# Kernel optimization log

Hardware: AMD Instinct MI355X
Metric: run time of the kernel (lower is better)

Reference implementation:

```python
import jax, jax.numpy as jnp
import numpy as np

C = 64          # num_channels
NB = 8          # num_bessel
NE = 10         # num_elements
N_NODES = 20000
N_EDGES = 320000

def _silu_norm():
    # e3nn normalize2mom constant for silu: 1/sqrt(E[silu(Z)^2]), Z~N(0,1)
    x, w = np.polynomial.hermite.hermgauss(100)
    z = np.sqrt(2.0) * x
    f = z / (1.0 + np.exp(-z))
    m2 = float(np.sum(w * f * f) / np.sqrt(np.pi))
    return np.float32(1.0 / np.sqrt(m2))

C_SILU = _silu_norm()
SQRT3 = np.float32(np.sqrt(3.0))
SQRT2 = np.float32(np.sqrt(2.0))
INV_SQRT_C = np.float32(1.0 / np.sqrt(C))
INV_SQRT_2C = np.float32(1.0 / np.sqrt(2 * C))
INV_SQRT_3C = np.float32(1.0 / np.sqrt(3 * C))
INV_SQRT_NB = np.float32(1.0 / np.sqrt(NB))
INV_SQRT_64 = np.float32(1.0 / np.sqrt(64.0))


def setup_inputs() -> dict:
    key = jax.random.key(0)
    ks = jax.random.split(key, 22)
    n = lambda k, s: jax.random.normal(k, s, dtype=jnp.float32)
    return {
        "node_feats": n(ks[0], (N_NODES, 4 * C)),
        "edge_feats": jax.random.uniform(ks[1], (N_EDGES, NB), dtype=jnp.float32),
        "edge_attrs": n(ks[2], (N_EDGES, 4)),
        "iedges": jax.random.randint(ks[3], (N_EDGES,), 0, N_NODES),
        "jedges": jax.random.randint(ks[4], (N_EDGES,), 0, N_NODES),
        "atomic_numbers": jax.random.randint(ks[5], (N_NODES,), 0, NE),
        "Wup0": n(ks[6], (C, C)), "Wup1": n(ks[7], (C, C)),
        "Wm1": n(ks[8], (NB, 64)), "Wm2": n(ks[9], (64, 64)),
        "Wm3": n(ks[10], (64, 64)), "Wm4": n(ks[11], (64, 5 * C)),
        "Wl0": n(ks[12], (2 * C, C)), "Wl1": n(ks[13], (3 * C, C)),
        "Ws0c1": n(ks[14], (NE, 1, C)), "Ws0c2": n(ks[15], (NE, 2, C)),
        "Ws0c3": n(ks[16], (NE, 2, C)),
        "Ws1c1": n(ks[17], (NE, 1, C)), "Ws1c2": n(ks[18], (NE, 1, C)),
        "Ws1c3": n(ks[19], (NE, 2, C)),
        "Wp0": n(ks[20], (C, C)), "Wp1": n(ks[21], (C, C)),
    }


def reference(node_feats, edge_feats, edge_attrs, iedges, jedges, atomic_numbers,
              Wup0, Wup1, Wm1, Wm2, Wm3, Wm4, Wl0, Wl1,
              Ws0c1, Ws0c2, Ws0c3, Ws1c1, Ws1c2, Ws1c3, Wp0, Wp1):
    Nn = node_feats.shape[0]
    # split irreps: C scalars (0e) then C vectors (1e), channel-major layout
    s = node_feats[:, :C]                       # (N, C)
    v = node_feats[:, C:].reshape(Nn, C, 3)     # (N, C, 3)

    # linear_up: per-l channel mixing, fan-in normalized (e3nn o3.Linear)
    s = (s @ Wup0) * INV_SQRT_C
    v = jnp.einsum('ncm,ck->nkm', v, Wup1) * INV_SQRT_C

    # conv_tp_weights: e3nn FullyConnectedNet [8,64,64,64,5C] with silu
    h = jax.nn.silu(edge_feats @ (Wm1 * INV_SQRT_NB)) * C_SILU
    h = jax.nn.silu(h @ (Wm2 * INV_SQRT_64)) * C_SILU
    h = jax.nn.silu(h @ (Wm3 * INV_SQRT_64)) * C_SILU
    tpw = h @ (Wm4 * INV_SQRT_64)               # (E, 5C)

    # gather sender node features per edge
    xs = s[iedges]                              # (E, C)
    xv = v[iedges]                              # (E, C, 3)
    eas = edge_attrs[:, 0:1]                    # (E, 1) scalar edge attr
    eav = edge_attrs[:, 1:4]                    # (E, 3) vector edge attr

    # 5 uvu CG paths (component-normalized e3nn TensorProduct):
    wa, wb = tpw[:, 0:C], tpw[:, C:2 * C]
    wc, wd, we = tpw[:, 2 * C:3 * C], tpw[:, 3 * C:4 * C], tpw[:, 4 * C:5 * C]
    m0 = wa * xs * eas                                              # 0e x 0e -> 0e
    m1 = wb * jnp.einsum('ecm,em->ec', xv, eav) / SQRT3             # 1e x 1e -> 0e
    m2 = (wc * xs)[:, :, None] * eav[:, None, :]                    # 0e x 1e -> 1e
    m3 = (wd * eas)[:, :, None] * xv                                # 1e x 0e -> 1e
    m4 = we[:, :, None] * jnp.cross(xv, eav[:, None, :]) / SQRT2    # 1e x 1e -> 1e

    # scatter-sum messages to receiver nodes
    msg_s = jax.ops.segment_sum(jnp.concatenate([m0, m1], axis=1), jedges, num_segments=Nn)        # (N, 2C)
    msg_v = jax.ops.segment_sum(jnp.concatenate([m2, m3, m4], axis=1), jedges, num_segments=Nn)    # (N, 3C, 3)

    # linear: middle irreps (2C x 0e + 3C x 1e) -> C x (0e + 1e)
    s2 = (msg_s @ Wl0) * INV_SQRT_2C            # (N, C)
    v2 = jnp.einsum('ncm,ck->nkm', msg_v, Wl1) * INV_SQRT_3C  # (N, C, 3)

    # symmetric (ACE/MACE) contraction, correlation=3, element-dependent weights
    w01 = Ws0c1[atomic_numbers, 0]              # (N, C)
    w02 = Ws0c2[atomic_numbers]                 # (N, 2, C)
    w03 = Ws0c3[atomic_numbers]                 # (N, 2, C)
    w11 = Ws1c1[atomic_numbers, 0]
    w12 = Ws1c2[atomic_numbers, 0]
    w13 = Ws1c3[atomic_numbers]
    vv = jnp.sum(v2 * v2, axis=-1)              # (N, C) = |v|^2 per channel
    out_s = (w01 * s2 + w02[:, 0] * s2 * s2 + w02[:, 1] * vv / SQRT3
             + w03[:, 0] * s2 * s2 * s2 + w03[:, 1] * s2 * vv / SQRT3)
    coef_v = w11 + w12 * s2 + w13[:, 0] * s2 * s2 + w13[:, 1] * vv / SQRT3
    out_v = coef_v[:, :, None] * v2             # (N, C, 3)

    # linearproduct
    so = (out_s @ Wp0) * INV_SQRT_C
    vo = jnp.einsum('ncm,ck->nkm', out_v, Wp1) * INV_SQRT_C
    return jnp.concatenate([so, vo.reshape(Nn, 3 * C)], axis=1)   # (N, 4C)
```

## Files before the change

### kernel.cpp

```cpp
#include <hip/hip_runtime.h>


typedef unsigned short u16;
typedef unsigned int u32;
typedef __attribute__((ext_vector_type(8))) short bf16x8;
typedef __attribute__((ext_vector_type(4))) float f32x4;

#define CW_UP0 0
#define CW_UP1 4096
#define CW_M1  8192
#define CW_M2  8704
#define CW_M3  12800
#define CW_M4  16896
#define CW_L0  37376
#define CW_L1  45568
#define CW_P0  57856
#define CW_P1  61952
#define CW_S01 66048
#define CW_S02 66688
#define CW_S03 67968
#define CW_S11 69248
#define CW_S12 69888
#define CW_S13 70528
#define CW_TOTAL 71808

#define C_SILU     1.6765224f
#define INV_SQRT3  0.57735027f
#define INV_SQRT2  0.70710678f
#define SC_L1      0.35355339f
#define SC_L234    0.125f

#define HS16 72
#define NFRAG 116
#define FW0 60
#define FW1 76
#define FP0 100
#define FP1 108
#define TP 88

__device__ __forceinline__ float b2f(u16 u) {
  union { u32 i; float f; } x; x.i = ((u32)u) << 16; return x.f;
}
__device__ __forceinline__ u16 f2b(float f) {
  union { float f; u32 i; } x; x.f = f;
  u32 i = x.i;
  u32 r = (i + 0x7fffu + ((i >> 16) & 1u)) >> 16;
  return (u16)r;
}
__device__ __forceinline__ float ldf(const void* p, size_t i, int f32) {
  return f32 ? ((const float*)p)[i] : b2f(((const u16*)p)[i]);
}
__device__ __forceinline__ float silu_n(float x) {
  return C_SILU * x / (1.0f + __expf(-x));
}

__global__ void k_detect(const void* nf, int* flag) {
  __shared__ int cnt;
  if (threadIdx.x == 0) cnt = 0;
  __syncthreads();
  const u16* p = (const u16*)nf;
  int wild = 0;
  for (int i = threadIdx.x; i < 4096; i += 256) {
    float ax = fabsf(b2f(p[i]));
    if (!(ax <= 1e10f) || (ax != 0.f && ax < 1e-10f)) wild++;
  }
  atomicAdd(&cnt, wild);
  __syncthreads();
  if (threadIdx.x == 0) *flag = (cnt > 100) ? 1 : 0;
}

struct WPtrs { const void* p[16]; };

__global__ __launch_bounds__(256) void k_front(
    WPtrs wp, float* __restrict__ cw, u16* __restrict__ bwH,
    u16* __restrict__ bwL, const int* __restrict__ je, int* __restrict__ deg,
    const void* __restrict__ nf, float* __restrict__ sup,
    float* __restrict__ vup, int nN, int nE, int nb0,
    const int* __restrict__ flagp) {
  __shared__ float row[4][256];
  const int f32 = *flagp;
  int bid = blockIdx.x, tid = threadIdx.x;

  if (bid < 281) {
    const int   sizes[16]  = {4096,4096,512,4096,4096,20480,8192,12288,4096,
                              4096,640,1280,1280,640,640,1280};
    const float scales[16] = {0.125f,0.125f,0.35355339f,0.125f,0.125f,0.125f,
                              0.08838835f,0.07216878f,0.125f,0.125f,
                              1.f,1.f,1.f,1.f,1.f,1.f};
    int gid = bid * 256 + tid;
    if (gid >= CW_TOTAL) return;
    int off = gid, seg = 0;
    while (off >= sizes[seg]) { off -= sizes[seg]; seg++; }
    cw[gid] = ldf(wp.p[seg], off, f32) * scales[seg];
  } else if (bid < 513) {
    int gid = (bid - 281) * 256 + tid;
    int f = gid >> 9, idx = gid & 511;
    int l = idx >> 3, j = idx & 7;
    int q = l >> 4, col16 = l & 15;
    float v = 0.f;
    if (f < 4) {
      int k = q * 8 + j, n = f * 16 + col16;
      if (k < 8) v = ldf(wp.p[2], (size_t)k * 64 + n, f32);
    } else if (f < 20) {
      const void* w = (f < 12) ? wp.p[3] : wp.p[4];
      int t = (f < 12) ? f - 4 : f - 12;
      int n = (t >> 1) * 16 + col16, ks = t & 1;
      int k = ks * 32 + q * 8 + j;
      v = ldf(w, (size_t)k * 64 + n, f32);
    } else if (f < 60) {
      int t = f - 20;
      int n = (t >> 1) * 16 + col16, ks = t & 1;
      int k = ks * 32 + q * 8 + j;
      v = ldf(wp.p[5], (size_t)k * 320 + n, f32);
    } else if (f < 76) {
      int t = f - FW0, ks = t >> 2, n = t & 3;
      int k = ks * 32 + q * 8 + j;
      v = ldf(wp.p[6], (size_t)k * 64 + n * 16 + col16, f32) * 0.08838835f;
    } else if (f < 100) {
      int t = f - FW1, ks = t >> 2, n = t & 3;
      int k = ks * 32 + q * 8 + j;
      v = ldf(wp.p[7], (size_t)k * 64 + n * 16 + col16, f32) * 0.07216878f;
    } else if (f < 108) {
      int t = f - FP0, ks = t >> 2, n = t & 3;
      int k = ks * 32 + q * 8 + j;
      v = ldf(wp.p[8], (size_t)k * 64 + n * 16 + col16, f32) * 0.125f;
    } else {
      int t = f - FP1, ks = t >> 2, n = t & 3;
      int k = ks * 32 + q * 8 + j;
      v = ldf(wp.p[9], (size_t)k * 64 + n * 16 + col16, f32) * 0.125f;
    }
    u16 hi = f2b(v);
    u16 lo = f2b(v - b2f(hi));
    size_t o = (size_t)f * 512 + (size_t)l * 8 + j;
    bwH[o] = hi;
    bwL[o] = lo;
  } else if (bid < nb0) {
    int e = (bid - 513) * 256 + tid;
    if (e < nE) atomicAdd(&deg[je[e]], 1);
  } else {
    int w = tid >> 6, l = tid & 63;
    int n = (bid - nb0) * 4 + w;
    bool valid = n < nN;
    int nn = valid ? n : 0;
#pragma unroll
    for (int t = 0; t < 4; t++)
      row[w][t * 64 + l] = ldf(nf, (size_t)nn * 256 + t * 64 + l, f32);
    __syncthreads();
    float sacc = 0.f, v0 = 0.f, v1 = 0.f, v2 = 0.f;
#pragma unroll 8
    for (int c = 0; c < 64; c++) {
      float w0 = ldf(wp.p[0], (size_t)c * 64 + l, f32);
      float w1 = ldf(wp.p[1], (size_t)c * 64 + l, f32);
      sacc += row[w][c] * w0;
      v0 += row[w][64 + c * 3 + 0] * w1;
      v1 += row[w][64 + c * 3 + 1] * w1;
      v2 += row[w][64 + c * 3 + 2] * w1;
    }
    if (valid) {
      sup[(size_t)n * 64 + l] = sacc * 0.125f;
      vup[((size_t)n * 3 + 0) * 64 + l] = v0 * 0.125f;
      vup[((size_t)n * 3 + 1) * 64 + l] = v1 * 0.125f;
      vup[((size_t)n * 3 + 2) * 64 + l] = v2 * 0.125f;
    }
  }
}

__global__ __launch_bounds__(256) void k_scan(const int* __restrict__ deg,
                                              int* __restrict__ offs,
                                              int* __restrict__ cursor, int nN) {
  __shared__ int part[256];
  int t = threadIdx.x;
  int per = (nN + 255) / 256;
  int lo = t * per, hi = (t + 1) * per; if (hi > nN) hi = nN;
  int s = 0;
  for (int i = lo; i < hi; i++) s += deg[i];
  part[t] = s;
  __syncthreads();
  if (t == 0) {
    int run = 0;
    for (int i = 0; i < 256; i++) { int v = part[i]; part[i] = run; run += v; }
    offs[nN] = run;
  }
  __syncthreads();
  int run = part[t];
  for (int i = lo; i < hi; i++) {
    offs[i] = run; cursor[i] = run; run += deg[i];
  }
}

__global__ __launch_bounds__(256) void k_scatter2(
    const int* __restrict__ je, const int* __restrict__ ie,
    const void* __restrict__ ea, const void* __restrict__ ef,
    int* __restrict__ cursor, int* __restrict__ iSlot,
    float4* __restrict__ eaSlot, float4* __restrict__ efSlot, int nE,
    const int* __restrict__ flagp) {
  const int f32 = *flagp;
  int e = blockIdx.x * 256 + threadIdx.x;
  if (e >= nE) return;
  int pos = atomicAdd(&cursor[je[e]], 1);
  iSlot[pos] = ie[e];
  float4 av;
  float4 f0, f1;
  if (f32) {
    av = ((const float4*)ea)[e];
    f0 = ((const float4*)ef)[(size_t)e * 2];
    f1 = ((const float4*)ef)[(size_t)e * 2 + 1];
  } else {
    uint2 r = ((const uint2*)ea)[e];
    av = make_float4(b2f(r.x & 0xffff), b2f(r.x >> 16),
                     b2f(r.y & 0xffff), b2f(r.y >> 16));
    uint4 u = ((const uint4*)ef)[e];
    f0 = make_float4(b2f(u.x & 0xffff), b2f(u.x >> 16),
                     b2f(u.y & 0xffff), b2f(u.y >> 16));
    f1 = make_float4(b2f(u.z & 0xffff), b2f(u.z >> 16),
                     b2f(u.w & 0xffff), b2f(u.w >> 16));
  }
  eaSlot[pos] = av;
  efSlot[(size_t)pos * 2] = f0;
  efSlot[(size_t)pos * 2 + 1] = f1;
}

__global__ __launch_bounds__(192) void k_mlp4(
    const float4* __restrict__ efSlot, const int* __restrict__ offs,
    const u16* __restrict__ bwH, const u16* __restrict__ bwL,
    u16* __restrict__ tpw, int gn0, int gn1, int capEff) {
  __shared__ u16 H[3][64 * HS16];
  int tid = threadIdx.x;
  int w = tid >> 6, l = tid & 63;
  int m = l & 15, q = l >> 4;
  int base = offs[gn0];
  int cnt = offs[gn1] - base;
  int lim = cnt < capEff ? cnt : capEff;
  int tb = (blockIdx.x * 3 + w) * 64;
  if (tb >= lim) return;
  u16* Hw = H[w];

  bf16x8 zero8 = {0,0,0,0,0,0,0,0};
  bf16x8 A1h[4], A1l[4];
#pragma unroll
  for (int t = 0; t < 4; t++) { A1h[t] = zero8; A1l[t] = zero8; }
  if (q == 0) {
#pragma unroll
    for (int t = 0; t < 4; t++) {
      int s = tb + t * 16 + m; if (s > lim - 1) s = lim - 1;
      float4 q0 = efSlot[((size_t)(base + s)) * 2];
      float4 q1 = efSlot[((size_t)(base + s)) * 2 + 1];
      float v[8] = {q0.x, q0.y, q0.z, q0.w, q1.x, q1.y, q1.z, q1.w};
      bf16x8 hi, lo;
#pragma unroll
      for (int j = 0; j < 8; j++) {
        u16 h = f2b(v[j]);
        hi[j] = (short)h;
        lo[j] = (short)f2b(v[j] - b2f(h));
      }
      A1h[t] = hi; A1l[t] = lo;
    }
  }
#pragma unroll
  for (int n = 0; n < 4; n++) {
    bf16x8 Bh = *(const bf16x8*)(bwH + (size_t)n * 512 + (size_t)l * 8);
    bf16x8 Bl = *(const bf16x8*)(bwL + (size_t)n * 512 + (size_t)l * 8);
#pragma unroll
    for (int t = 0; t < 4; t++) {
      f32x4 c = (f32x4){0.f, 0.f, 0.f, 0.f};
      c = __builtin_amdgcn_mfma_f32_16x16x32_bf16(A1h[t], Bh, c, 0, 0, 0);
      c = __builtin_amdgcn_mfma_f32_16x16x32_bf16(A1l[t], Bh, c, 0, 0, 0);
      c = __builtin_amdgcn_mfma_f32_16x16x32_bf16(A1h[t], Bl, c, 0, 0, 0);
#pragma unroll
      for (int r = 0; r < 4; r++)
        Hw[(t * 16 + q * 4 + r) * HS16 + n * 16 + m] =
            f2b(silu_n(c[r] * SC_L1));
    }
  }

#pragma unroll
  for (int layer = 0; layer < 2; layer++) {
    int fragBase = 4 + layer * 8;
    bf16x8 Ah[2][4];
#pragma unroll
    for (int ks = 0; ks < 2; ks++)
#pragma unroll
      for (int t = 0; t < 4; t++)
        Ah[ks][t] = *(const bf16x8*)(Hw + (t * 16 + m) * HS16 + ks * 32 + q * 8);
#pragma unroll
    for (int n = 0; n < 4; n++) {
      bf16x8 B0h = *(const bf16x8*)(bwH + (size_t)(fragBase + n * 2 + 0) * 512 +
                                    (size_t)l * 8);
      bf16x8 B0l = *(const bf16x8*)(bwL + (size_t)(fragBase + n * 2 + 0) * 512 +
                                    (size_t)l * 8);
      bf16x8 B1h = *(const bf16x8*)(bwH + (size_t)(fragBase + n * 2 + 1) * 512 +
                                    (size_t)l * 8);
      bf16x8 B1l = *(const bf16x8*)(bwL + (size_t)(fragBase + n * 2 + 1) * 512 +
                                    (size_t)l * 8);
#pragma unroll
      for (int t = 0; t < 4; t++) {
        f32x4 c = (f32x4){0.f, 0.f, 0.f, 0.f};
        c = __builtin_amdgcn_mfma_f32_16x16x32_bf16(Ah[0][t], B0h, c, 0, 0, 0);
        c = __builtin_amdgcn_mfma_f32_16x16x32_bf16(Ah[0][t], B0l, c, 0, 0, 0);
        c = __builtin_amdgcn_mfma_f32_16x16x32_bf16(Ah[1][t], B1h, c, 0, 0, 0);
        c = __builtin_amdgcn_mfma_f32_16x16x32_bf16(Ah[1][t], B1l, c, 0, 0, 0);
#pragma unroll
        for (int r = 0; r < 4; r++)
          Hw[(t * 16 + q * 4 + r) * HS16 + n * 16 + m] =
              f2b(silu_n(c[r] * SC_L234));
      }
    }
  }

  {
    bf16x8 Ah[2][4];
#pragma unroll
    for (int ks = 0; ks < 2; ks++)
#pragma unroll
      for (int t = 0; t < 4; t++)
        Ah[ks][t] = *(const bf16x8*)(Hw + (t * 16 + m) * HS16 + ks * 32 + q * 8);
    for (int c4 = 0; c4 < 5; c4++) {
#pragma unroll
      for (int nn2 = 0; nn2 < 4; nn2++) {
        int n = c4 * 4 + nn2;
        bf16x8 B0h = *(const bf16x8*)(bwH + (size_t)(20 + n * 2 + 0) * 512 +
                                      (size_t)l * 8);
        bf16x8 B0l = *(const bf16x8*)(bwL + (size_t)(20 + n * 2 + 0) * 512 +
                                      (size_t)l * 8);
        bf16x8 B1h = *(const bf16x8*)(bwH + (size_t)(20 + n * 2 + 1) * 512 +
                                      (size_t)l * 8);
        bf16x8 B1l = *(const bf16x8*)(bwL + (size_t)(20 + n * 2 + 1) * 512 +
                                      (size_t)l * 8);
#pragma unroll
        for (int t = 0; t < 4; t++) {
          f32x4 c = (f32x4){0.f, 0.f, 0.f, 0.f};
          c = __builtin_amdgcn_mfma_f32_16x16x32_bf16(Ah[0][t], B0h, c, 0, 0, 0);
          c = __builtin_amdgcn_mfma_f32_16x16x32_bf16(Ah[0][t], B0l, c, 0, 0, 0);
          c = __builtin_amdgcn_mfma_f32_16x16x32_bf16(Ah[1][t], B1h, c, 0, 0, 0);
          c = __builtin_amdgcn_mfma_f32_16x16x32_bf16(Ah[1][t], B1l, c, 0, 0, 0);
#pragma unroll
          for (int r = 0; r < 4; r++)
            Hw[(t * 16 + q * 4 + r) * HS16 + nn2 * 16 + m] =
                f2b(c[r] * SC_L234);
        }
      }
      int r8 = l >> 3, cc = l & 7;
#pragma unroll
      for (int i = 0; i < 8; i++) {
        int row = i * 8 + r8;
        int srow = tb + row;
        if (srow < lim) {
          uint4 v = *(const uint4*)(Hw + row * HS16 + cc * 8);
          *(uint4*)(tpw + (size_t)srow * 320 + c4 * 64 + cc * 8) = v;
        }
      }
    }
  }
}

__global__ __launch_bounds__(256) void k_gather6(
    const int* __restrict__ iSlot, const float4* __restrict__ eaSlot,
    const int* __restrict__ offs, const float* __restrict__ sup,
    const float* __restrict__ vup, const u16* __restrict__ tpw,
    u16* __restrict__ msgSh, u16* __restrict__ msgSl,
    u16* __restrict__ msgVh, u16* __restrict__ msgVl,
    int gn0, int gn1, int capEff) {
  int w = threadIdx.x >> 6, l = threadIdx.x & 63;
  int n = gn0 + blockIdx.x * 4 + w;
  if (n >= gn1) return;
  int gbase = offs[gn0];
  int start = offs[n];
  int deg = offs[n + 1] - start;
  int avail = capEff - (start - gbase);
  int dmax = deg < avail ? deg : avail;
  if (dmax < 0) dmax = 0;

  float as0 = 0.f, as1 = 0.f;
  float av[9];
#pragma unroll
  for (int m = 0; m < 9; m++) av[m] = 0.f;

  for (int c0 = 0; c0 < dmax; c0 += 64) {
    int rem = dmax - c0;
    int cend = rem < 64 ? rem : 64;
    int iA = 0;
    float4 eaA = make_float4(0.f, 0.f, 0.f, 0.f);
    if (l < cend) {
      iA = iSlot[start + c0 + l];
      eaA = eaSlot[start + c0 + l];
    }
    for (int qq = 0; qq < cend; qq++) {
      int i = __shfl(iA, qq);
      float eas = __shfl(eaA.x, qq);
      float ev0 = __shfl(eaA.y, qq);
      float ev1 = __shfl(eaA.z, qq);
      float ev2 = __shfl(eaA.w, qq);
      const u16* tp = tpw + (size_t)(start - gbase + c0 + qq) * 320;
      float wa  = b2f(tp[l]);
      float wbv = b2f(tp[64 + l]);
      float wc  = b2f(tp[128 + l]);
      float wd  = b2f(tp[192 + l]);
      float we_ = b2f(tp[256 + l]);
      float xs  = sup[(size_t)i * 64 + l];
      float xv0 = vup[((size_t)i * 3 + 0) * 64 + l];
      float xv1 = vup[((size_t)i * 3 + 1) * 64 + l];
      float xv2 = vup[((size_t)i * 3 + 2) * 64 + l];
      float dot = xv0 * ev0 + xv1 * ev1 + xv2 * ev2;
      as0 += wa * xs * eas;
      as1 += wbv * dot * INV_SQRT3;
      float wcxs = wc * xs;
      float wde  = wd * eas;
      float wef  = we_ * INV_SQRT2;
      av[0] += wcxs * ev0; av[1] += wcxs * ev1; av[2] += wcxs * ev2;
      av[3] += wde * xv0;  av[4] += wde * xv1;  av[5] += wde * xv2;
      av[6] += wef * (xv1 * ev2 - xv2 * ev1);
      av[7] += wef * (xv2 * ev0 - xv0 * ev2);
      av[8] += wef * (xv0 * ev1 - xv1 * ev0);
    }
  }

  {
    u16 h0 = f2b(as0), h1 = f2b(as1);
    msgSh[(size_t)n * 128 + l] = h0;
    msgSh[(size_t)n * 128 + 64 + l] = h1;
    msgSl[(size_t)n * 128 + l] = f2b(as0 - b2f(h0));
    msgSl[(size_t)n * 128 + 64 + l] = f2b(as1 - b2f(h1));
  }
#pragma unroll
  for (int c = 0; c < 3; c++) {
#pragma unroll
    for (int b = 0; b < 3; b++) {
      float x = av[b * 3 + c];
      u16 h = f2b(x);
      size_t o = (size_t)n * 576 + c * 192 + b * 64 + l;
      msgVh[o] = h;
      msgVl[o] = f2b(x - b2f(h));
    }
  }
}

__global__ __launch_bounds__(256) void k_post2(
    const u16* __restrict__ msgSh, const u16* __restrict__ msgSl,
    const u16* __restrict__ msgVh, const u16* __restrict__ msgVl,
    const int* __restrict__ an, const float* __restrict__ cw,
    const u16* __restrict__ bwH, const u16* __restrict__ bwL,
    void* __restrict__ out, int nN, const int* __restrict__ flagp) {
  __shared__ u16 Thi[16][TP];
  __shared__ u16 Tlo[16][TP];
  const int f32 = *flagp;
  int tid = threadIdx.x;
  int w = tid >> 6, l = tid & 63;
  int m = l & 15, q = l >> 4;
  int n0 = blockIdx.x * 16;
  int rowA = n0 + m; if (rowA > nN - 1) rowA = nN - 1;

  f32x4 s2 = (f32x4){0.f, 0.f, 0.f, 0.f};
#pragma unroll
  for (int ks = 0; ks < 4; ks++) {
    bf16x8 Bh = *(const bf16x8*)(bwH + (size_t)(FW0 + ks * 4 + w) * 512 +
                                 (size_t)l * 8);
    bf16x8 Bl = *(const bf16x8*)(bwL + (size_t)(FW0 + ks * 4 + w) * 512 +
                                 (size_t)l * 8);
    bf16x8 Ah = *(const bf16x8*)(msgSh + (size_t)rowA * 128 + ks * 32 + q * 8);
    bf16x8 Al = *(const bf16x8*)(msgSl + (size_t)rowA * 128 + ks * 32 + q * 8);
    s2 = __builtin_amdgcn_mfma_f32_16x16x32_bf16(Ah, Bh, s2, 0, 0, 0);
    s2 = __builtin_amdgcn_mfma_f32_16x16x32_bf16(Al, Bh, s2, 0, 0, 0);
    s2 = __builtin_amdgcn_mfma_f32_16x16x32_bf16(Ah, Bl, s2, 0, 0, 0);
  }

  f32x4 v2[3];
#pragma unroll
  for (int c = 0; c < 3; c++) v2[c] = (f32x4){0.f, 0.f, 0.f, 0.f};
#pragma unroll
  for (int ks = 0; ks < 6; ks++) {
    bf16x8 Bh = *(const bf16x8*)(bwH + (size_t)(FW1 + ks * 4 + w) * 512 +
                                 (size_t)l * 8);
    bf16x8 Bl = *(const bf16x8*)(bwL + (size_t)(FW1 + ks * 4 + w) * 512 +
                                 (size_t)l * 8);
#pragma unroll
    for (int c = 0; c < 3; c++) {
      size_t o = (size_t)rowA * 576 + c * 192 + ks * 32 + q * 8;
      bf16x8 Ah = *(const bf16x8*)(msgVh + o);
      bf16x8 Al = *(const bf16x8*)(msgVl + o);
      v2[c] = __builtin_amdgcn_mfma_f32_16x16x32_bf16(Ah, Bh, v2[c], 0, 0, 0);
      v2[c] = __builtin_amdgcn_mfma_f32_16x16x32_bf16(Al, Bh, v2[c], 0, 0, 0);
      v2[c] = __builtin_amdgcn_mfma_f32_16x16x32_bf16(Ah, Bl, v2[c], 0, 0, 0);
    }
  }

  float os[4], ov0[4], ov1[4], ov2[4];
#pragma unroll
  for (int r = 0; r < 4; r++) {
    int node = n0 + q * 4 + r;
    int nc = node > nN - 1 ? nN - 1 : node;
    int a = an[nc];
    int ch = w * 16 + m;
    float s2v = s2[r];
    float va = v2[0][r], vb = v2[1][r], vc = v2[2][r];
    float vv = va * va + vb * vb + vc * vc;
    float w01  = cw[CW_S01 + a * 64 + ch];
    float w02a = cw[CW_S02 + a * 128 + ch];
    float w02b = cw[CW_S02 + a * 128 + 64 + ch];
    float w03a = cw[CW_S03 + a * 128 + ch];
    float w03b = cw[CW_S03 + a * 128 + 64 + ch];
    float w11  = cw[CW_S11 + a * 64 + ch];
    float w12  = cw[CW_S12 + a * 64 + ch];
    float w13a = cw[CW_S13 + a * 128 + ch];
    float w13b = cw[CW_S13 + a * 128 + 64 + ch];
    float s2sq = s2v * s2v;
    float vvs = vv * INV_SQRT3;
    os[r] = w01 * s2v + w02a * s2sq + w02b * vvs + w03a * s2sq * s2v +
            w03b * s2v * vvs;
    float coef = w11 + w12 * s2v + w13a * s2sq + w13b * vvs;
    ov0[r] = coef * va;
    ov1[r] = coef * vb;
    ov2[r] = coef * vc;
  }

#define POST2_G2(SRC, FB, STORE_S, COMP)                                       \
  {                                                                            \
    __syncthreads();                                                           \
    _Pragma("unroll")                                                          \
    for (int r = 0; r < 4; r++) {                                              \
      float x = SRC[r];                                                        \
      u16 h = f2b(x);                                                          \
      Thi[q * 4 + r][w * 16 + m] = h;                                          \
      Tlo[q * 4 + r][w * 16 + m] = f2b(x - b2f(h));                            \
    }                                                                          \
    __syncthreads();                                                           \
    f32x4 d = (f32x4){0.f, 0.f, 0.f, 0.f};                                     \
    _Pragma("unroll")                                                          \
    for (int ks = 0; ks < 2; ks++) {                                           \
      bf16x8 Bh = *(const bf16x8*)(bwH + (size_t)(FB + ks * 4 + w) * 512 +     \
                                   (size_t)l * 8);                             \
      bf16x8 Bl = *(const bf16x8*)(bwL + (size_t)(FB + ks * 4 + w) * 512 +     \
                                   (size_t)l * 8);                             \
      bf16x8 Ah = *(const bf16x8*)(&Thi[m][ks * 32 + q * 8]);                  \
      bf16x8 Al = *(const bf16x8*)(&Tlo[m][ks * 32 + q * 8]);                  \
      d = __builtin_amdgcn_mfma_f32_16x16x32_bf16(Ah, Bh, d, 0, 0, 0);         \
      d = __builtin_amdgcn_mfma_f32_16x16x32_bf16(Al, Bh, d, 0, 0, 0);         \
      d = __builtin_amdgcn_mfma_f32_16x16x32_bf16(Ah, Bl, d, 0, 0, 0);         \
    }                                                                          \
    _Pragma("unroll")                                                          \
    for (int r = 0; r < 4; r++) {                                              \
      int node = n0 + q * 4 + r;                                               \
      if (node < nN) {                                                         \
        int ch = w * 16 + m;                                                   \
        size_t basep = (size_t)node * 256;                                     \
        size_t oidx = STORE_S ? (basep + ch) : (basep + 64 + ch * 3 + COMP);   \
        if (f32) ((float*)out)[oidx] = d[r];                                   \
        else ((u16*)out)[oidx] = f2b(d[r]);                                    \
      }                                                                        \
    }                                                                          \
  }

  POST2_G2(os, FP0, 1, 0)
  POST2_G2(ov0, FP1, 0, 0)
  POST2_G2(ov1, FP1, 0, 1)
  POST2_G2(ov2, FP1, 0, 2)
#undef POST2_G2
}

extern "C" void kernel_launch(void* const* d_in, const int* in_sizes, int n_in,
                              void* d_out, int out_size, void* d_ws,
                              size_t ws_size, hipStream_t stream) {
  const void* nf = d_in[0];
  const void* ef = d_in[1];
  const void* ea = d_in[2];
  const int* ie = (const int*)d_in[3];
  const int* je = (const int*)d_in[4];
  const int* an = (const int*)d_in[5];
  int nN = in_sizes[0] / 256;
  int nE = in_sizes[3];

  size_t intCnt = (size_t)3 * nN + 1 + nE;
  intCnt = (intCnt + 3) & ~(size_t)3;
  int* deg    = (int*)d_ws;
  int* offs   = deg + nN;
  int* cursor = offs + nN + 1;
  int* iSlot  = cursor + nN;
  float* cw   = (float*)d_ws + intCnt;
  float* sup  = cw + CW_TOTAL;
  float* vup  = sup + (size_t)nN * 64;
  int* flag   = (int*)(vup + (size_t)nN * 192);

  size_t msgByte = (size_t)((char*)(flag + 1) - (char*)d_ws);
  msgByte = (msgByte + 15) & ~(size_t)15;
  u16* msgSh = (u16*)((char*)d_ws + msgByte);
  u16* msgSl = msgSh + (size_t)nN * 128;
  u16* msgVh = msgSl + (size_t)nN * 128;
  u16* msgVl = msgVh + (size_t)nN * 576;

  size_t eaByte = msgByte + (size_t)nN * 1408 * 2;
  eaByte = (eaByte + 15) & ~(size_t)15;
  float4* eaSlot = (float4*)((char*)d_ws + eaByte);
  float4* efSlot = eaSlot + nE;
  size_t bwByte = eaByte + (size_t)nE * 16 + (size_t)nE * 32;
  u16* bwH = (u16*)((char*)d_ws + bwByte);
  u16* bwL = bwH + (size_t)NFRAG * 512;
  size_t tpwByte = bwByte + (size_t)NFRAG * 512 * 2 * 2;
  tpwByte = (tpwByte + 15) & ~(size_t)15;
  u16* tpw = (u16*)((char*)d_ws + tpwByte);
  size_t capE = (ws_size > tpwByte) ? (ws_size - tpwByte) / 640 : 0;

  int G = 64;
  int nodesPer = (nN + 63) / 64;
  for (int g = 1; g <= 64; g++) {
    int npg = (nN + g - 1) / g;
    size_t worst = (size_t)npg * nE / nN + 6000;
    if (worst <= capE) { G = g; nodesPer = npg; break; }
  }
  int capEff = (int)((size_t)nodesPer * nE / nN + 6000);
  if ((size_t)capEff > capE) capEff = (int)capE;

  k_detect<<<1, 256, 0, stream>>>(nf, flag);
  hipMemsetAsync(deg, 0, (size_t)nN * sizeof(int), stream);

  WPtrs wp;
  const int widx[16] = {6, 7, 8, 9, 10, 11, 12, 13, 20, 21,
                        14, 15, 16, 17, 18, 19};
  for (int i = 0; i < 16; i++) wp.p[i] = d_in[widx[i]];

  int histNB = (nE + 255) / 256;
  int nb0 = 513 + histNB;
  int nupNB = (nN + 3) / 4;
  k_front<<<nb0 + nupNB, 256, 0, stream>>>(wp, cw, bwH, bwL, je, deg, nf,
                                           sup, vup, nN, nE, nb0, flag);
  k_scan<<<1, 256, 0, stream>>>(deg, offs, cursor, nN);
  k_scatter2<<<(nE + 255) / 256, 256, 0, stream>>>(je, ie, ea, ef, cursor,
                                                   iSlot, eaSlot, efSlot, nE,
                                                   flag);

  for (int g = 0; g < G; g++) {
    int gn0 = g * nodesPer;
    if (gn0 >= nN) break;
    int gn1 = gn0 + nodesPer; if (gn1 > nN) gn1 = nN;
    int mlpBlocks = (capEff + 191) / 192;
    k_mlp4<<<mlpBlocks, 192, 0, stream>>>(efSlot, offs, bwH, bwL, tpw,
                                          gn0, gn1, capEff);
    int gBlocks = (gn1 - gn0 + 3) / 4;
    k_gather6<<<gBlocks, 256, 0, stream>>>(iSlot, eaSlot, offs, sup, vup,
                                           tpw, msgSh, msgSl, msgVh, msgVl,
                                           gn0, gn1, capEff);
  }
  int postNB = (nN + 15) / 16;
  k_post2<<<postNB, 256, 0, stream>>>(msgSh, msgSl, msgVh, msgVl, an, cw,
                                      bwH, bwL, d_out, nN, flag);
}
```

Measured before the change: 500.2 us.

## Fold degree zeroing into detect, stage up-weights in LDS, parallelize scan

Zeroing of the degree array moves into the single-block detect kernel, which removes one memset launch. The linear_up weight matrices are staged into shared memory once per block instead of being read from global memory inside the channel loop. The serial per-thread prefix scan is replaced by a chunked wave-shuffle scan that gives coalesced access. In exchange, k_front now uses about 32KB more LDS per block (which may reduce occupancy), and every block, including the weight-conversion and histogram blocks, declares it. The single-block detect also now zeroes 20k ints on its own.

```diff
diff --git a/kernel.cpp b/kernel.cpp
--- a/kernel.cpp
+++ b/kernel.cpp
@@ -54,7 +54,7 @@
   return C_SILU * x / (1.0f + __expf(-x));
 }
 
-__global__ void k_detect(const void* nf, int* flag) {
+__global__ void k_detect(const void* nf, int* flag, int* deg, int nN) {
   __shared__ int cnt;
   if (threadIdx.x == 0) cnt = 0;
   __syncthreads();
@@ -65,6 +65,7 @@
     if (!(ax <= 1e10f) || (ax != 0.f && ax < 1e-10f)) wild++;
   }
   atomicAdd(&cnt, wild);
+  for (int i = threadIdx.x; i < nN; i += 256) deg[i] = 0;
   __syncthreads();
   if (threadIdx.x == 0) *flag = (cnt > 100) ? 1 : 0;
 }
@@ -78,6 +79,8 @@
     float* __restrict__ vup, int nN, int nE, int nb0,
     const int* __restrict__ flagp) {
   __shared__ float row[4][256];
+  __shared__ float w0s[4096];
+  __shared__ float w1s[4096];
   const int f32 = *flagp;
   int bid = blockIdx.x, tid = threadIdx.x;
 
@@ -143,14 +146,19 @@
     bool valid = n < nN;
     int nn = valid ? n : 0;
 #pragma unroll
+    for (int i = 0; i < 16; i++) {
+      w0s[i * 256 + tid] = ldf(wp.p[0], i * 256 + tid, f32);
+      w1s[i * 256 + tid] = ldf(wp.p[1], i * 256 + tid, f32);
+    }
+#pragma unroll
     for (int t = 0; t < 4; t++)
       row[w][t * 64 + l] = ldf(nf, (size_t)nn * 256 + t * 64 + l, f32);
     __syncthreads();
     float sacc = 0.f, v0 = 0.f, v1 = 0.f, v2 = 0.f;
 #pragma unroll 8
     for (int c = 0; c < 64; c++) {
-      float w0 = ldf(wp.p[0], (size_t)c * 64 + l, f32);
-      float w1 = ldf(wp.p[1], (size_t)c * 64 + l, f32);
+      float w0 = w0s[c * 64 + l];
+      float w1 = w1s[c * 64 + l];
       sacc += row[w][c] * w0;
       v0 += row[w][64 + c * 3 + 0] * w1;
       v1 += row[w][64 + c * 3 + 1] * w1;
@@ -168,24 +176,34 @@
 __global__ __launch_bounds__(256) void k_scan(const int* __restrict__ deg,
                                               int* __restrict__ offs,
                                               int* __restrict__ cursor, int nN) {
-  __shared__ int part[256];
+  __shared__ int wsum[8];
   int t = threadIdx.x;
-  int per = (nN + 255) / 256;
-  int lo = t * per, hi = (t + 1) * per; if (hi > nN) hi = nN;
-  int s = 0;
-  for (int i = lo; i < hi; i++) s += deg[i];
-  part[t] = s;
-  __syncthreads();
-  if (t == 0) {
-    int run = 0;
-    for (int i = 0; i < 256; i++) { int v = part[i]; part[i] = run; run += v; }
-    offs[nN] = run;
-  }
-  __syncthreads();
-  int run = part[t];
-  for (int i = lo; i < hi; i++) {
-    offs[i] = run; cursor[i] = run; run += deg[i];
-  }
+  int lane = t & 63, wv = t >> 6;
+  int base = 0;
+  for (int c0 = 0; c0 < nN; c0 += 256) {
+    int i = c0 + t;
+    int v = (i < nN) ? deg[i] : 0;
+    int s = v;
+#pragma unroll
+    for (int off = 1; off < 64; off <<= 1) {
+      int x = __shfl_up(s, off);
+      if (lane >= off) s += x;
+    }
+    if (lane == 63) wsum[wv] = s;
+    __syncthreads();
+    if (t == 0) {
+      int r = 0;
+#pragma unroll
+      for (int ww = 0; ww < 4; ww++) { int x = wsum[ww]; wsum[ww] = r; r += x; }
+      wsum[4] = r;
+    }
+    __syncthreads();
+    int excl = base + wsum[wv] + s - v;
+    if (i < nN) { offs[i] = excl; cursor[i] = excl; }
+    base += wsum[4];
+    __syncthreads();
+  }
+  if (t == 0) offs[nN] = base;
 }
 
 __global__ __launch_bounds__(256) void k_scatter2(
@@ -608,8 +626,7 @@
   int capEff = (int)((size_t)nodesPer * nE / nN + 6000);
   if ((size_t)capEff > capE) capEff = (int)capE;
 
-  k_detect<<<1, 256, 0, stream>>>(nf, flag);
-  hipMemsetAsync(deg, 0, (size_t)nN * sizeof(int), stream);
+  k_detect<<<1, 256, 0, stream>>>(nf, flag, deg, nN);
 
   WPtrs wp;
   const int widx[16] = {6, 7, 8, 9, 10, 11, 12, 13, 20, 21,
```

After: 536.3 us. +7.2%, slower.
